# Kernel tuning notes

Hardware: AMD Instinct MI355X
Metric: run time of the kernel (lower is better)

Reference implementation:

```python
import jax, jax.numpy as jnp
import numpy as np

B, D, H, O, E = 4096, 1024, 4096, 1024, 8
TOP_K = 2


def setup_inputs() -> dict:
    key = jax.random.key(0)
    ks = jax.random.split(key, 7)
    s = 0.02
    return {
        "expert_input": jax.random.normal(ks[0], (B, D), dtype=jnp.float32),
        "Wg": jax.random.normal(ks[1], (D, E), dtype=jnp.float32) * s,
        "bg": jnp.zeros((E,), dtype=jnp.float32),
        "W1": jax.random.normal(ks[2], (E, D, H), dtype=jnp.float32) * s,
        "b1": jnp.zeros((E, H), dtype=jnp.float32),
        "W2": jax.random.normal(ks[3], (E, H, O), dtype=jnp.float32) * s,
        "b2": jnp.zeros((E, O), dtype=jnp.float32),
    }


def reference(expert_input, Wg, bg, W1, b1, W2, b2):
    x = expert_input                                  # [B, D]
    gate_logits = x @ Wg + bg                         # [B, E]
    topk_logits, topk_idx = jax.lax.top_k(gate_logits, TOP_K)
    topk_w = jax.nn.softmax(topk_logits, axis=1)      # softmax over the k selected logits
    rows = jnp.arange(x.shape[0])[:, None]
    dense_w = jnp.zeros_like(gate_logits).at[rows, topk_idx].set(topk_w)  # [B, E]
    # Dense (all-experts) evaluation; zero gate weight == unrouted, so math
    # matches the masked per-expert loop in the torch module exactly.
    h = jax.nn.relu(jnp.einsum('bd,edh->ebh', x, W1) + b1[:, None, :])    # [E, B, H]
    expert_out = jnp.einsum('ebh,eho->ebo', h, W2) + b2[:, None, :]       # [E, B, O]
    routed = jnp.einsum('be,ebo->bo', dense_w, expert_out)                # [B, O]
    return routed
```

## Files before the change

kernel.cpp:

```cpp
#include <hip/hip_runtime.h>
#include <cstdint>

#define DEVI __device__ __forceinline__

typedef __bf16 bf16x8_t __attribute__((ext_vector_type(8)));
typedef float f32x4_t __attribute__((ext_vector_type(4)));

typedef const __attribute__((address_space(1))) unsigned int* gas_t;
typedef __attribute__((address_space(3))) unsigned int* las_t;

DEVI void glds16(const void* g, void* l) {
  __builtin_amdgcn_global_load_lds((gas_t)g, (las_t)l, 16, 0, 0);
}

DEVI uint16_t f2b(float f) {
  uint32_t u = __builtin_bit_cast(uint32_t, f);
  u += 0x7fffu + ((u >> 16) & 1u);
  return (uint16_t)(u >> 16);
}

static constexpr int MAXT = 72;

__global__ __launch_bounds__(256) void moe_gate(const float* __restrict__ x,
    const float* __restrict__ Wg, const float* __restrict__ bg,
    int* __restrict__ gidx, float* __restrict__ gw) {
  const int lane = threadIdx.x & 63;
  const int b = blockIdx.x * 4 + (threadIdx.x >> 6);
  float acc[8];
#pragma unroll
  for (int e = 0; e < 8; ++e) acc[e] = 0.f;
  const float* xr = x + (size_t)b * 1024;
#pragma unroll
  for (int it = 0; it < 4; ++it) {
    const int d0 = it * 256 + lane * 4;
    float4 xv = *(const float4*)(xr + d0);
    float xs[4] = {xv.x, xv.y, xv.z, xv.w};
#pragma unroll
    for (int q = 0; q < 4; ++q) {
      const float4* wrow = (const float4*)(Wg + (size_t)(d0 + q) * 8);
      float4 wa = wrow[0], wb = wrow[1];
      acc[0] += xs[q] * wa.x; acc[1] += xs[q] * wa.y;
      acc[2] += xs[q] * wa.z; acc[3] += xs[q] * wa.w;
      acc[4] += xs[q] * wb.x; acc[5] += xs[q] * wb.y;
      acc[6] += xs[q] * wb.z; acc[7] += xs[q] * wb.w;
    }
  }
#pragma unroll
  for (int off = 32; off; off >>= 1)
#pragma unroll
    for (int e = 0; e < 8; ++e) acc[e] += __shfl_xor(acc[e], off, 64);
  if (lane == 0) {
    float l[8];
#pragma unroll
    for (int e = 0; e < 8; ++e) l[e] = acc[e] + bg[e];
    int i0 = 0;
#pragma unroll
    for (int e = 1; e < 8; ++e) if (l[e] > l[i0]) i0 = e;
    int i1 = (i0 == 0) ? 1 : 0;
#pragma unroll
    for (int e = 0; e < 8; ++e) if (e != i0 && l[e] > l[i1]) i1 = e;
    float ex = expf(l[i1] - l[i0]);
    float s = 1.f + ex;
    gidx[2 * b] = i0; gidx[2 * b + 1] = i1;
    gw[2 * b] = 1.f / s; gw[2 * b + 1] = ex / s;
  }
}

__global__ __launch_bounds__(256) void moe_scan(const int* __restrict__ gidx,
                                                int* __restrict__ meta) {
  __shared__ int cnt[8];
  if (threadIdx.x < 8) cnt[threadIdx.x] = 0;
  __syncthreads();
  int loc[8] = {0, 0, 0, 0, 0, 0, 0, 0};
  for (int i = threadIdx.x; i < 8192; i += 256) {
    int e = gidx[i];
#pragma unroll
    for (int q = 0; q < 8; ++q) loc[q] += (e == q) ? 1 : 0;
  }
#pragma unroll
  for (int q = 0; q < 8; ++q) atomicAdd(&cnt[q], loc[q]);
  __syncthreads();
  if (threadIdx.x == 0) {
    int off = 0, t = 0;
    for (int e = 0; e < 8; ++e) {
      int c = cnt[e];
      meta[e] = c;
      meta[8 + e] = off;
      meta[17 + e] = 0;
      int nt = (c + 127) >> 7;
      for (int mt = 0; mt < nt; ++mt) {
        meta[32 + t] = e;
        meta[104 + t] = off + mt * 128;
        meta[176 + t] = off + c;
        ++t;
      }
      off += c;
    }
    meta[16] = off;
    meta[25] = t;
  }
}

__global__ __launch_bounds__(256) void moe_scatter(const int* __restrict__ gidx,
    const float* __restrict__ gw, int* __restrict__ meta,
    int* __restrict__ row_index, float* __restrict__ row_w) {
  int i = blockIdx.x * 256 + threadIdx.x;
  int e = gidx[i];
  int pos = meta[8 + e] + atomicAdd(&meta[17 + e], 1);
  row_index[pos] = i >> 1;
  row_w[pos] = gw[i];
}

__global__ __launch_bounds__(256) void moe_cvtx(const float* __restrict__ x,
                                                uint16_t* __restrict__ xb) {
  size_t i = ((size_t)blockIdx.x * 256 + threadIdx.x) * 4;
  float4 v = *(const float4*)(x + i);
  uint64_t pk = (uint64_t)f2b(v.x) | ((uint64_t)f2b(v.y) << 16) |
                ((uint64_t)f2b(v.z) << 32) | ((uint64_t)f2b(v.w) << 48);
  *(uint64_t*)(xb + i) = pk;
}

__global__ __launch_bounds__(256) void moe_transpose(const float* __restrict__ in,
                                                     uint16_t* __restrict__ outp,
                                                     int K, int N) {
  __shared__ uint16_t t[64][72];
  const int e = blockIdx.z;
  const int k0 = blockIdx.y * 64, n0 = blockIdx.x * 64;
  const int r = threadIdx.x >> 2;
  const int c0 = (threadIdx.x & 3) * 16;
  const float* src = in + ((size_t)e * K + k0 + r) * N + n0 + c0;
#pragma unroll
  for (int q = 0; q < 4; ++q) {
    float4 v = *(const float4*)(src + q * 4);
    uint64_t pk = (uint64_t)f2b(v.x) | ((uint64_t)f2b(v.y) << 16) |
                  ((uint64_t)f2b(v.z) << 32) | ((uint64_t)f2b(v.w) << 48);
    *(uint64_t*)&t[r][c0 + q * 4] = pk;
  }
  __syncthreads();
  alignas(16) uint16_t buf[16];
#pragma unroll
  for (int j = 0; j < 16; ++j) buf[j] = t[c0 + j][r];
  uint16_t* dst = outp + ((size_t)e * N + n0 + r) * K + k0 + c0;
  *(uint4*)dst = *(const uint4*)&buf[0];
  *(uint4*)(dst + 8) = *(const uint4*)&buf[8];
}

template <int KD, int ND, int MODE>
__global__ __launch_bounds__(256, 4) void moe_gemm(
    const uint16_t* __restrict__ Am, const uint16_t* __restrict__ Bt,
    const float* __restrict__ bias, const int* __restrict__ meta,
    const int* __restrict__ row_index, const float* __restrict__ row_w,
    uint16_t* __restrict__ hout, float* __restrict__ out) {
  constexpr int NB = ND / 128;
  const int nwg = gridDim.x;
  const int orig = blockIdx.x;
  const int q8 = nwg >> 3, r8 = nwg & 7, xcd = orig & 7, loc = orig >> 3;
  int wg = (xcd < r8 ? xcd * (q8 + 1) : r8 * (q8 + 1) + (xcd - r8) * q8) + loc;
  const int nb = wg % NB;
  const int ty = wg / NB;
  if (ty >= meta[25]) return;
  const int e = meta[32 + ty];
  const int pos0 = meta[104 + ty];
  const int vend = meta[176 + ty];

  __shared__ uint16_t As[2][128 * 32];
  __shared__ uint16_t Bs[2][128 * 32];

  const int tid = threadIdx.x;
  const int lane = tid & 63;
  const int w = tid >> 6;
  const int wr = w >> 1, wc = w & 1;

  size_t aoff[2], boff[2];
#pragma unroll
  for (int j = 0; j < 2; ++j) {
    int c = j * 256 + tid;
    int row = c >> 2;
    int skc = (c & 3) ^ ((row >> 1) & 3);
    int pos = pos0 + row;
    if (pos > 8191) pos = 8191;
    int ar = (MODE == 1) ? row_index[pos] : pos;
    aoff[j] = ((size_t)ar * KD + (size_t)skc * 8) * 2;
    boff[j] = (((size_t)e * ND + (size_t)nb * 128 + row) * KD + (size_t)skc * 8) * 2;
  }
  const char* Ag = (const char*)Am;
  const char* Bg = (const char*)Bt;

  f32x4_t acc[4][4];
  f32x4_t z;
  z[0] = 0.f; z[1] = 0.f; z[2] = 0.f; z[3] = 0.f;
#pragma unroll
  for (int m = 0; m < 4; ++m)
#pragma unroll
    for (int n = 0; n < 4; ++n) acc[m][n] = z;

  auto stage = [&](int buf, int t) {
#pragma unroll
    for (int j = 0; j < 2; ++j) {
      glds16(Ag + aoff[j] + (size_t)t * 64, &As[buf][(j * 256 + w * 64) * 8]);
      glds16(Bg + boff[j] + (size_t)t * 64, &Bs[buf][(j * 256 + w * 64) * 8]);
    }
  };

  stage(0, 0);
  __syncthreads();
  int cur = 0;
  const int NIT = KD / 32;
  for (int t = 0; t < NIT; ++t) {
    if (t + 1 < NIT) stage(cur ^ 1, t + 1);
    const uint16_t* Ap = As[cur];
    const uint16_t* Bp = Bs[cur];
    bf16x8_t af[4], bfr[4];
#pragma unroll
    for (int m = 0; m < 4; ++m) {
      int row = wr * 64 + m * 16 + (lane & 15);
      int skc = ((lane >> 4) ^ (row >> 1)) & 3;
      af[m] = *(const bf16x8_t*)(Ap + row * 32 + skc * 8);
    }
#pragma unroll
    for (int n = 0; n < 4; ++n) {
      int row = wc * 64 + n * 16 + (lane & 15);
      int skc = ((lane >> 4) ^ (row >> 1)) & 3;
      bfr[n] = *(const bf16x8_t*)(Bp + row * 32 + skc * 8);
    }
#pragma unroll
    for (int m = 0; m < 4; ++m)
#pragma unroll
      for (int n = 0; n < 4; ++n)
        acc[m][n] = __builtin_amdgcn_mfma_f32_16x16x32_bf16(af[m], bfr[n], acc[m][n], 0, 0, 0);
    __syncthreads();
    cur ^= 1;
  }

  const int cb = nb * 128 + wc * 64;
  if constexpr (MODE == 1) {
#pragma unroll
    for (int m = 0; m < 4; ++m) {
      int pr = pos0 + wr * 64 + m * 16 + ((lane >> 4) << 2);
#pragma unroll
      for (int i = 0; i < 4; ++i) {
        int pos = pr + i;
        if (pos < vend) {
#pragma unroll
          for (int n = 0; n < 4; ++n) {
            int col = cb + n * 16 + (lane & 15);
            float v = acc[m][n][i] + bias[e * ND + col];
            v = fmaxf(v, 0.f);
            hout[(size_t)pos * ND + col] = f2b(v);
          }
        }
      }
    }
  } else {
#pragma unroll
    for (int m = 0; m < 4; ++m) {
      int pr = pos0 + wr * 64 + m * 16 + ((lane >> 4) << 2);
#pragma unroll
      for (int i = 0; i < 4; ++i) {
        int pos = pr + i;
        if (pos < vend) {
          int bi = row_index[pos];
          float wgt = row_w[pos];
          float* orow = out + (size_t)bi * ND;
#pragma unroll
          for (int n = 0; n < 4; ++n) {
            int col = cb + n * 16 + (lane & 15);
            float v = (acc[m][n][i] + bias[e * ND + col]) * wgt;
            atomicAdd(orow + col, v);
          }
        }
      }
    }
  }
}

extern "C" void kernel_launch(void* const* d_in, const int* in_sizes, int n_in,
                              void* d_out, int out_size, void* d_ws, size_t ws_size,
                              hipStream_t stream) {
  const float* x  = (const float*)d_in[0];
  const float* Wg = (const float*)d_in[1];
  const float* bg = (const float*)d_in[2];
  const float* W1 = (const float*)d_in[3];
  const float* b1 = (const float*)d_in[4];
  const float* W2 = (const float*)d_in[5];
  const float* b2 = (const float*)d_in[6];
  float* out = (float*)d_out;

  char* ws = (char*)d_ws;
  uint16_t* w1t = (uint16_t*)ws; ws += (size_t)8 * 4096 * 1024 * 2;
  uint16_t* w2t = (uint16_t*)ws; ws += (size_t)8 * 1024 * 4096 * 2;
  uint16_t* xb  = (uint16_t*)ws; ws += (size_t)4096 * 1024 * 2;
  uint16_t* h   = (uint16_t*)ws; ws += (size_t)8192 * 4096 * 2;
  int*   gidx = (int*)ws;   ws += 8192 * 4;
  float* gw   = (float*)ws; ws += 8192 * 4;
  int*   rix  = (int*)ws;   ws += 8192 * 4;
  float* rw   = (float*)ws; ws += 8192 * 4;
  int*   meta = (int*)ws;   ws += 4096;

  hipMemsetAsync(d_out, 0, (size_t)4096 * 1024 * 4, stream);
  moe_cvtx<<<4096, 256, 0, stream>>>(x, xb);
  moe_transpose<<<dim3(4096 / 64, 1024 / 64, 8), 256, 0, stream>>>(W1, w1t, 1024, 4096);
  moe_transpose<<<dim3(1024 / 64, 4096 / 64, 8), 256, 0, stream>>>(W2, w2t, 4096, 1024);
  moe_gate<<<1024, 256, 0, stream>>>(x, Wg, bg, gidx, gw);
  moe_scan<<<1, 256, 0, stream>>>(gidx, meta);
  moe_scatter<<<32, 256, 0, stream>>>(gidx, gw, meta, rix, rw);
  moe_gemm<1024, 4096, 1><<<dim3(32 * MAXT), 256, 0, stream>>>(xb, w1t, b1, meta, rix, rw, h, nullptr);
  moe_gemm<4096, 1024, 2><<<dim3(8 * MAXT), 256, 0, stream>>>(h, w2t, b2, meta, rix, rw, nullptr, out);
}
```

Baseline: 431.7 us.

## Merge prep kernels and overlap W2 transpose with first expert GEMM

Folds the x-to-bf16 conversion into the gate kernel and runs the W1 transpose blocks in the same launch. Merges scan and scatter into one single-block kernel. Appends the W2 transpose blocks to the first expert GEMM launch so that work can fill idle CUs, with a simplified XCD remap. This cuts launch count and per-launch tail gaps. In exchange, the scatter now runs in a single block, and the transpose blocks are pinned to the GEMM's launch bounds and LDS footprint.

```diff
diff --git a/kernel.cpp b/kernel.cpp
--- a/kernel.cpp
+++ b/kernel.cpp
@@ -21,19 +21,24 @@
 
 static constexpr int MAXT = 72;
 
-__global__ __launch_bounds__(256) void moe_gate(const float* __restrict__ x,
-    const float* __restrict__ Wg, const float* __restrict__ bg,
-    int* __restrict__ gidx, float* __restrict__ gw) {
+DEVI void gate_body(int bid, const float* __restrict__ x,
+                    const float* __restrict__ Wg, const float* __restrict__ bg,
+                    int* __restrict__ gidx, float* __restrict__ gw,
+                    uint16_t* __restrict__ xb) {
   const int lane = threadIdx.x & 63;
-  const int b = blockIdx.x * 4 + (threadIdx.x >> 6);
+  const int b = bid * 4 + (threadIdx.x >> 6);
   float acc[8];
 #pragma unroll
   for (int e = 0; e < 8; ++e) acc[e] = 0.f;
   const float* xr = x + (size_t)b * 1024;
+  uint16_t* xbr = xb + (size_t)b * 1024;
 #pragma unroll
   for (int it = 0; it < 4; ++it) {
     const int d0 = it * 256 + lane * 4;
     float4 xv = *(const float4*)(xr + d0);
+    uint64_t pk = (uint64_t)f2b(xv.x) | ((uint64_t)f2b(xv.y) << 16) |
+                  ((uint64_t)f2b(xv.z) << 32) | ((uint64_t)f2b(xv.w) << 48);
+    *(uint64_t*)(xbr + d0) = pk;
     float xs[4] = {xv.x, xv.y, xv.z, xv.w};
 #pragma unroll
     for (int q = 0; q < 4; ++q) {
@@ -66,66 +71,9 @@
   }
 }
 
-__global__ __launch_bounds__(256) void moe_scan(const int* __restrict__ gidx,
-                                                int* __restrict__ meta) {
-  __shared__ int cnt[8];
-  if (threadIdx.x < 8) cnt[threadIdx.x] = 0;
-  __syncthreads();
-  int loc[8] = {0, 0, 0, 0, 0, 0, 0, 0};
-  for (int i = threadIdx.x; i < 8192; i += 256) {
-    int e = gidx[i];
-#pragma unroll
-    for (int q = 0; q < 8; ++q) loc[q] += (e == q) ? 1 : 0;
-  }
-#pragma unroll
-  for (int q = 0; q < 8; ++q) atomicAdd(&cnt[q], loc[q]);
-  __syncthreads();
-  if (threadIdx.x == 0) {
-    int off = 0, t = 0;
-    for (int e = 0; e < 8; ++e) {
-      int c = cnt[e];
-      meta[e] = c;
-      meta[8 + e] = off;
-      meta[17 + e] = 0;
-      int nt = (c + 127) >> 7;
-      for (int mt = 0; mt < nt; ++mt) {
-        meta[32 + t] = e;
-        meta[104 + t] = off + mt * 128;
-        meta[176 + t] = off + c;
-        ++t;
-      }
-      off += c;
-    }
-    meta[16] = off;
-    meta[25] = t;
-  }
-}
-
-__global__ __launch_bounds__(256) void moe_scatter(const int* __restrict__ gidx,
-    const float* __restrict__ gw, int* __restrict__ meta,
-    int* __restrict__ row_index, float* __restrict__ row_w) {
-  int i = blockIdx.x * 256 + threadIdx.x;
-  int e = gidx[i];
-  int pos = meta[8 + e] + atomicAdd(&meta[17 + e], 1);
-  row_index[pos] = i >> 1;
-  row_w[pos] = gw[i];
-}
-
-__global__ __launch_bounds__(256) void moe_cvtx(const float* __restrict__ x,
-                                                uint16_t* __restrict__ xb) {
-  size_t i = ((size_t)blockIdx.x * 256 + threadIdx.x) * 4;
-  float4 v = *(const float4*)(x + i);
-  uint64_t pk = (uint64_t)f2b(v.x) | ((uint64_t)f2b(v.y) << 16) |
-                ((uint64_t)f2b(v.z) << 32) | ((uint64_t)f2b(v.w) << 48);
-  *(uint64_t*)(xb + i) = pk;
-}
-
-__global__ __launch_bounds__(256) void moe_transpose(const float* __restrict__ in,
-                                                     uint16_t* __restrict__ outp,
-                                                     int K, int N) {
-  __shared__ uint16_t t[64][72];
-  const int e = blockIdx.z;
-  const int k0 = blockIdx.y * 64, n0 = blockIdx.x * 64;
+DEVI void transpose_body(const float* __restrict__ in, uint16_t* __restrict__ outp,
+                         int K, int N, int e, int k0, int n0,
+                         uint16_t (*t)[72]) {
   const int r = threadIdx.x >> 2;
   const int c0 = (threadIdx.x & 3) * 16;
   const float* src = in + ((size_t)e * K + k0 + r) * N + n0 + c0;
@@ -145,26 +93,81 @@
   *(uint4*)(dst + 8) = *(const uint4*)&buf[8];
 }
 
+__global__ __launch_bounds__(256) void moe_m1(const float* __restrict__ x,
+    const float* __restrict__ Wg, const float* __restrict__ bg,
+    int* __restrict__ gidx, float* __restrict__ gw, uint16_t* __restrict__ xb,
+    const float* __restrict__ W1, uint16_t* __restrict__ w1t) {
+  __shared__ uint16_t t[64][72];
+  const int bid = blockIdx.x;
+  if (bid < 1024) {
+    gate_body(bid, x, Wg, bg, gidx, gw, xb);
+  } else {
+    int tt = bid - 1024;
+    int e = tt >> 10, rem = tt & 1023;
+    int kb = rem >> 6, nb2 = rem & 63;
+    transpose_body(W1, w1t, 1024, 4096, e, kb * 64, nb2 * 64, t);
+  }
+}
+
+__global__ __launch_bounds__(256) void moe_scan2(const int* __restrict__ gidx,
+    const float* __restrict__ gw, int* __restrict__ meta,
+    int* __restrict__ row_index, float* __restrict__ row_w) {
+  __shared__ int cnt[8];
+  __shared__ int offs[8];
+  __shared__ int fill[8];
+  if (threadIdx.x < 8) { cnt[threadIdx.x] = 0; fill[threadIdx.x] = 0; }
+  __syncthreads();
+  int loc[8] = {0, 0, 0, 0, 0, 0, 0, 0};
+  for (int i = threadIdx.x; i < 8192; i += 256) {
+    int e = gidx[i];
+#pragma unroll
+    for (int q = 0; q < 8; ++q) loc[q] += (e == q) ? 1 : 0;
+  }
+#pragma unroll
+  for (int q = 0; q < 8; ++q) if (loc[q]) atomicAdd(&cnt[q], loc[q]);
+  __syncthreads();
+  if (threadIdx.x == 0) {
+    int off = 0, tIdx = 0;
+    for (int e = 0; e < 8; ++e) {
+      int c = cnt[e];
+      meta[e] = c;
+      meta[8 + e] = off;
+      offs[e] = off;
+      int nt = (c + 127) >> 7;
+      for (int mt = 0; mt < nt; ++mt) {
+        meta[32 + tIdx] = e;
+        meta[104 + tIdx] = off + mt * 128;
+        meta[176 + tIdx] = off + c;
+        ++tIdx;
+      }
+      off += c;
+    }
+    meta[16] = off;
+    meta[25] = tIdx;
+  }
+  __syncthreads();
+  for (int i = threadIdx.x; i < 8192; i += 256) {
+    int e = gidx[i];
+    int pos = offs[e] + atomicAdd(&fill[e], 1);
+    row_index[pos] = i >> 1;
+    row_w[pos] = gw[i];
+  }
+}
+
 template <int KD, int ND, int MODE>
-__global__ __launch_bounds__(256, 4) void moe_gemm(
-    const uint16_t* __restrict__ Am, const uint16_t* __restrict__ Bt,
-    const float* __restrict__ bias, const int* __restrict__ meta,
-    const int* __restrict__ row_index, const float* __restrict__ row_w,
-    uint16_t* __restrict__ hout, float* __restrict__ out) {
+DEVI void gemm_core(int wg, const uint16_t* __restrict__ Am,
+                    const uint16_t* __restrict__ Bt, const float* __restrict__ bias,
+                    const int* __restrict__ meta, const int* __restrict__ row_index,
+                    const float* __restrict__ row_w, uint16_t* __restrict__ hout,
+                    float* __restrict__ out, uint16_t (*As)[4096], uint16_t (*Bs)[4096]) {
   constexpr int NB = ND / 128;
-  const int nwg = gridDim.x;
-  const int orig = blockIdx.x;
-  const int q8 = nwg >> 3, r8 = nwg & 7, xcd = orig & 7, loc = orig >> 3;
-  int wg = (xcd < r8 ? xcd * (q8 + 1) : r8 * (q8 + 1) + (xcd - r8) * q8) + loc;
+  constexpr int NIT = KD / 32;
   const int nb = wg % NB;
   const int ty = wg / NB;
   if (ty >= meta[25]) return;
   const int e = meta[32 + ty];
   const int pos0 = meta[104 + ty];
   const int vend = meta[176 + ty];
-
-  __shared__ uint16_t As[2][128 * 32];
-  __shared__ uint16_t Bs[2][128 * 32];
 
   const int tid = threadIdx.x;
   const int lane = tid & 63;
@@ -205,7 +208,6 @@
   stage(0, 0);
   __syncthreads();
   int cur = 0;
-  const int NIT = KD / 32;
   for (int t = 0; t < NIT; ++t) {
     if (t + 1 < NIT) stage(cur ^ 1, t + 1);
     const uint16_t* Ap = As[cur];
@@ -272,6 +274,41 @@
       }
     }
   }
+}
+
+__global__ __launch_bounds__(256, 4) void moe_m2(const uint16_t* __restrict__ xb,
+    const uint16_t* __restrict__ w1t, const float* __restrict__ b1,
+    const int* __restrict__ meta, const int* __restrict__ rix,
+    const float* __restrict__ rw, uint16_t* __restrict__ h,
+    const float* __restrict__ W2, uint16_t* __restrict__ w2t) {
+  __shared__ uint16_t As[2][4096];
+  __shared__ uint16_t Bs[2][4096];
+  const int bid = blockIdx.x;
+  if (bid < 2304) {
+    constexpr int NWG = 2304;
+    constexpr int Q8 = NWG >> 3;
+    int wg = (bid & 7) * Q8 + (bid >> 3);
+    gemm_core<1024, 4096, 1>(wg, xb, w1t, b1, meta, rix, rw, h, nullptr, As, Bs);
+  } else {
+    int tt = bid - 2304;
+    int e = tt >> 10, rem = tt & 1023;
+    int kb = rem >> 4, nb2 = rem & 15;
+    transpose_body(W2, w2t, 4096, 1024, e, kb * 64, nb2 * 64,
+                   (uint16_t(*)[72]) & As[0][0]);
+  }
+}
+
+__global__ __launch_bounds__(256, 4) void moe_gemm2(const uint16_t* __restrict__ h,
+    const uint16_t* __restrict__ w2t, const float* __restrict__ b2,
+    const int* __restrict__ meta, const int* __restrict__ rix,
+    const float* __restrict__ rw, float* __restrict__ out) {
+  __shared__ uint16_t As[2][4096];
+  __shared__ uint16_t Bs[2][4096];
+  const int nwg = gridDim.x;
+  const int orig = blockIdx.x;
+  const int q8 = nwg >> 3, r8 = nwg & 7, xcd = orig & 7, loc = orig >> 3;
+  int wg = (xcd < r8 ? xcd * (q8 + 1) : r8 * (q8 + 1) + (xcd - r8) * q8) + loc;
+  gemm_core<4096, 1024, 2>(wg, h, w2t, b2, meta, rix, rw, nullptr, out, As, Bs);
 }
 
 extern "C" void kernel_launch(void* const* d_in, const int* in_sizes, int n_in,
@@ -298,12 +335,8 @@
   int*   meta = (int*)ws;   ws += 4096;
 
   hipMemsetAsync(d_out, 0, (size_t)4096 * 1024 * 4, stream);
-  moe_cvtx<<<4096, 256, 0, stream>>>(x, xb);
-  moe_transpose<<<dim3(4096 / 64, 1024 / 64, 8), 256, 0, stream>>>(W1, w1t, 1024, 4096);
-  moe_transpose<<<dim3(1024 / 64, 4096 / 64, 8), 256, 0, stream>>>(W2, w2t, 4096, 1024);
-  moe_gate<<<1024, 256, 0, stream>>>(x, Wg, bg, gidx, gw);
-  moe_scan<<<1, 256, 0, stream>>>(gidx, meta);
-  moe_scatter<<<32, 256, 0, stream>>>(gidx, gw, meta, rix, rw);
-  moe_gemm<1024, 4096, 1><<<dim3(32 * MAXT), 256, 0, stream>>>(xb, w1t, b1, meta, rix, rw, h, nullptr);
-  moe_gemm<4096, 1024, 2><<<dim3(8 * MAXT), 256, 0, stream>>>(h, w2t, b2, meta, rix, rw, nullptr, out);
-}
+  moe_m1<<<dim3(1024 + 8192), 256, 0, stream>>>(x, Wg, bg, gidx, gw, xb, W1, w1t);
+  moe_scan2<<<dim3(1), 256, 0, stream>>>(gidx, gw, meta, rix, rw);
+  moe_m2<<<dim3(2304 + 8192), 256, 0, stream>>>(xb, w1t, b1, meta, rix, rw, h, W2, w2t);
+  moe_gemm2<<<dim3(8 * MAXT), 256, 0, stream>>>(h, w2t, b2, meta, rix, rw, out);
+}
```

Result: faster. 392.1 us (-9.2%).
